# Optimization experiments

Hardware: AMD Instinct MI355X
Metric: run time of the kernel (lower is better)

The kernel has to match this reference:

```python
import jax, jax.numpy as jnp
import numpy as np

T, B, D, H = 512, 64, 1024, 1024
SIGMA = 0.01

def setup_inputs() -> dict:
    key = jax.random.key(0)
    ks = jax.random.split(key, 10)
    w = lambda k, shape: jax.random.normal(k, shape, dtype=jnp.float32) * SIGMA
    return {
        "inputs": jax.random.normal(ks[0], (T, B, D), dtype=jnp.float32),
        "H0": jnp.zeros((B, H), dtype=jnp.float32),
        "C0": jnp.zeros((B, H), dtype=jnp.float32),
        "W_xi": w(ks[1], (D, H)), "W_hi": w(ks[2], (H, H)), "b_i": jnp.zeros((H,), jnp.float32),
        "W_xf": w(ks[3], (D, H)), "W_hf": w(ks[4], (H, H)), "b_f": jnp.zeros((H,), jnp.float32),
        "W_xo": w(ks[5], (D, H)), "W_ho": w(ks[6], (H, H)), "b_o": jnp.zeros((H,), jnp.float32),
        "W_xc": w(ks[7], (D, H)), "W_hc": w(ks[8], (H, H)), "b_c": jnp.zeros((H,), jnp.float32),
    }

def reference(inputs, H0, C0, W_xi, W_hi, b_i, W_xf, W_hf, b_f,
              W_xo, W_ho, b_o, W_xc, W_hc, b_c):
    # Precompute all input-side gate projections in one big GEMM over the
    # full sequence: [T, B, 4H]. Recurrent H-projection stays in the scan.
    Wx = jnp.concatenate([W_xi, W_xf, W_xo, W_xc], axis=1)   # [D, 4H]
    Wh = jnp.concatenate([W_hi, W_hf, W_ho, W_hc], axis=1)   # [H, 4H]
    b  = jnp.concatenate([b_i, b_f, b_o, b_c])                # [4H]
    x_proj = jnp.einsum('tbd,dh->tbh', inputs, Wx) + b        # [T, B, 4H]

    def step(carry, xg):
        h, c = carry
        gates = xg + h @ Wh                                   # [B, 4H]
        i, f, o, g = jnp.split(gates, 4, axis=-1)
        i = jax.nn.sigmoid(i); f = jax.nn.sigmoid(f); o = jax.nn.sigmoid(o)
        c_new = f * c + i * jnp.tanh(g)
        h_new = o * jnp.tanh(c_new)
        return (h_new, c_new), h_new

    (Hf, Cf), outputs = jax.lax.scan(step, (H0, C0), x_proj)
    return outputs, Hf, Cf
```

## Files before the change

### kernel.cpp

```cpp
#include <hip/hip_runtime.h>


typedef unsigned short u16;
typedef unsigned int   u32;
typedef unsigned long long u64;
typedef __attribute__((ext_vector_type(8))) short bf16x8;
typedef __attribute__((ext_vector_type(4))) float f32x4;

__device__ __forceinline__ float bf2f(u16 u) {
    union { u32 i; float f; } v; v.i = ((u32)u) << 16; return v.f;
}
__device__ __forceinline__ u16 f2bf(float f) {
    union { float f; u32 u; } v; v.f = f;
    u32 u = v.u;
    return (u16)((u + 0x7FFFu + ((u >> 16) & 1u)) >> 16);
}
__device__ __forceinline__ float sigm(float x)   { return 1.f / (1.f + __expf(-x)); }
__device__ __forceinline__ float tanh_f(float x) { return 1.f - 2.f / (1.f + __expf(2.f * x)); }

__global__ void k_init(const float* __restrict__ H0,
                       const float* __restrict__ bi, const float* __restrict__ bff,
                       const float* __restrict__ bo, const float* __restrict__ bc,
                       u16* __restrict__ hbuf, float* __restrict__ bias,
                       u32* __restrict__ flags)
{
    int i = blockIdx.x * 256 + threadIdx.x;
#pragma unroll
    for (int r = 0; r < 4; ++r) {
        int idx = i + r * 16384;
        hbuf[idx] = f2bf(H0[idx]);
    }
    if (i < 4096) {
        const float* bp = (i < 1024) ? bi : (i < 2048) ? bff : (i < 3072) ? bo : bc;
        bias[i] = bp[i & 1023];
    }
    if (i < 1024) flags[i] = 0u;
}

__global__ void k_cvt(const float4* __restrict__ in, ushort4* __restrict__ out)
{
    size_t i = (size_t)blockIdx.x * 256 + threadIdx.x;
    float4 v = in[i];
    ushort4 o;
    o.x = f2bf(v.x); o.y = f2bf(v.y); o.z = f2bf(v.z); o.w = f2bf(v.w);
    out[i] = o;
}

__global__ void k_wt(const float* s0, const float* s1, const float* s2, const float* s3,
                     const float* s4, const float* s5, const float* s6, const float* s7,
                     u16* __restrict__ wxT, u16* __restrict__ whT)
{
    const float* srcs[8] = {s0, s1, s2, s3, s4, s5, s6, s7};
    int z = blockIdx.z;
    const float* src = srcs[z];
    u16* dst = (z < 4) ? (wxT + (size_t)z * 1048576) : (whT + (size_t)(z - 4) * 1048576);
    __shared__ float tile[32][33];
    int k0 = blockIdx.x * 32, n0 = blockIdx.y * 32;
    int tx = threadIdx.x, ty = threadIdx.y;
#pragma unroll
    for (int s = 0; s < 4; ++s)
        tile[ty + 8 * s][tx] = src[(size_t)(k0 + ty + 8 * s) * 1024 + n0 + tx];
    __syncthreads();
#pragma unroll
    for (int s = 0; s < 4; ++s)
        dst[(size_t)(n0 + ty + 8 * s) * 1024 + k0 + tx] = f2bf(tile[tx][ty + 8 * s]);
}

__global__ __launch_bounds__(256, 2) void k_gemm(const u16* __restrict__ A,
                                                 const u16* __restrict__ BT,
                                                 u16* __restrict__ C)
{
    __shared__ __attribute__((aligned(16))) u16 lsA[128][64];
    __shared__ __attribute__((aligned(16))) u16 lsB[128][64];
    const int tid  = threadIdx.x;
    const int lane = tid & 63;
    const int wv   = tid >> 6;
    const int wm   = wv >> 1, wn = wv & 1;
    const int m0   = blockIdx.x * 128;
    const int n0   = blockIdx.y * 128;
    const int fr   = lane & 15, fq = lane >> 4;
    const int srow = tid >> 3;
    const int sk8  = tid & 7;

    f32x4 acc[4][4] = {};

    for (int kt = 0; kt < 16; ++kt) {
        const int k0 = kt * 64;
#pragma unroll
        for (int it = 0; it < 4; ++it) {
            int row = srow + it * 32;
            int kg  = (sk8 ^ (row & 7)) * 8;
            uint4 va = *(const uint4*)(A  + (size_t)(m0 + row) * 1024 + k0 + kg);
            uint4 vb = *(const uint4*)(BT + (size_t)(n0 + row) * 1024 + k0 + kg);
            *(uint4*)&lsA[row][sk8 * 8] = va;
            *(uint4*)&lsB[row][sk8 * 8] = vb;
        }
        __syncthreads();
#pragma unroll
        for (int kc = 0; kc < 2; ++kc) {
            const int kb = kc * 32 + 8 * fq;
            bf16x8 af[4], bfv[4];
#pragma unroll
            for (int i = 0; i < 4; ++i) {
                int ra = 64 * wm + 16 * i + fr;
                af[i] = *(const bf16x8*)&lsA[ra][kb ^ ((ra & 7) * 8)];
            }
#pragma unroll
            for (int j = 0; j < 4; ++j) {
                int rb = 64 * wn + 16 * j + fr;
                bfv[j] = *(const bf16x8*)&lsB[rb][kb ^ ((rb & 7) * 8)];
            }
#pragma unroll
            for (int i = 0; i < 4; ++i)
#pragma unroll
                for (int j = 0; j < 4; ++j)
                    acc[i][j] = __builtin_amdgcn_mfma_f32_16x16x32_bf16(af[i], bfv[j], acc[i][j], 0, 0, 0);
        }
        __syncthreads();
    }
#pragma unroll
    for (int i = 0; i < 4; ++i) {
        int grow = m0 + 64 * wm + 16 * i + 4 * fq;
#pragma unroll
        for (int j = 0; j < 4; ++j) {
            int gcol = n0 + 64 * wn + 16 * j + fr;
#pragma unroll
            for (int r = 0; r < 4; ++r)
                C[(size_t)(grow + r) * 4096 + gcol] = f2bf(acc[i][j][r]);
        }
    }
}

__global__ __launch_bounds__(512, 1) void k_scan(const u16* __restrict__ xproj,
                                                 const u16* __restrict__ whT,
                                                 const float* __restrict__ bias,
                                                 const float* __restrict__ C0,
                                                 u16* __restrict__ hbuf,
                                                 u32* __restrict__ flags,
                                                 float* __restrict__ out)
{
    __shared__ __attribute__((aligned(16))) u16   lds_w[64][1024];
    __shared__ __attribute__((aligned(16))) float lds_p[4][4][16][16];

    const int wg  = blockIdx.x;
    const int bg  = wg >> 6;
    const int cg  = wg & 63;
    const int b0  = bg * 16;
    const int j0  = cg * 16;
    const int tid = threadIdx.x;
    const int lane = tid & 63;
    const int wv  = tid >> 6;
    const int fr  = lane & 15;
    const int fq  = lane >> 4;

    for (int it = 0; it < 16; ++it) {
        int idx = tid + it * 512;
        int row = idx >> 7;
        int k8  = idx & 127;
        int gg  = row >> 4, jj = row & 15;
        uint4 v = *((const uint4*)(whT + ((size_t)(gg * 1024 + j0 + jj) << 10)) + k8);
        *(uint4*)&lds_w[row][(k8 * 8) ^ ((row & 7) * 8)] = v;
    }

    const int eb = tid >> 4;
    const int ej = tid & 15;
    float c_state = 0.f;
    float bia[4] = {0.f, 0.f, 0.f, 0.f};
    if (tid < 256) {
        c_state = C0[(size_t)(b0 + eb) * 1024 + j0 + ej];
#pragma unroll
        for (int q = 0; q < 4; ++q) bia[q] = bias[q * 1024 + j0 + ej];
    }
    __syncthreads();

    const int ks = wv;
    u32* fl = flags + bg * 256;

    for (int t = 0; t < 512; ++t) {
        const int p = t & 1;
        const u16* hb = hbuf + (size_t)p * 65536;

        union { bf16x8 v[4]; uint4 q[4]; } afu;
        {
            const u16* hp = hb + (size_t)(b0 + fr) * 1024 + ks * 128 + 8 * fq;
#pragma unroll
            for (int kk = 0; kk < 4; ++kk)
                afu.q[kk] = *(const uint4*)(hp + kk * 32);
        }

        float xg[4] = {0.f, 0.f, 0.f, 0.f};
        if (tid < 256) {
            const u16* xp = xproj + ((size_t)t * 64 + (b0 + eb)) * 4096 + j0 + ej;
#pragma unroll
            for (int q = 0; q < 4; ++q) xg[q] = bf2f(xp[q * 1024]);
        }

        f32x4 acc[4] = {};
#pragma unroll
        for (int g = 0; g < 4; ++g) {
            const int row = g * 16 + fr;
            const int swz = (row & 7) * 8;
#pragma unroll
            for (int kk = 0; kk < 4; ++kk) {
                bf16x8 bv = *(const bf16x8*)&lds_w[row][(ks * 128 + kk * 32 + 8 * fq) ^ swz];
                acc[g] = __builtin_amdgcn_mfma_f32_16x16x32_bf16(afu.v[kk], bv, acc[g], 0, 0, 0);
            }
        }

        if (wv >= 4) {
#pragma unroll
            for (int g = 0; g < 4; ++g)
#pragma unroll
                for (int r = 0; r < 4; ++r)
                    lds_p[wv - 4][g][4 * fq + r][fr] = acc[g][r];
        }
        __syncthreads();
        if (wv < 4) {
#pragma unroll
            for (int g = 0; g < 4; ++g)
#pragma unroll
                for (int r = 0; r < 4; ++r)
                    lds_p[wv][g][4 * fq + r][fr] += acc[g][r];
        }
        __syncthreads();

        if (tid < 256) {
            float gate[4];
#pragma unroll
            for (int q = 0; q < 4; ++q)
                gate[q] = lds_p[0][q][eb][ej] + lds_p[1][q][eb][ej]
                        + lds_p[2][q][eb][ej] + lds_p[3][q][eb][ej] + xg[q] + bia[q];
            float i_ = sigm(gate[0]);
            float f_ = sigm(gate[1]);
            float o_ = sigm(gate[2]);
            float g_ = tanh_f(gate[3]);
            c_state = f_ * c_state + i_ * g_;
            float h_ = o_ * tanh_f(c_state);

            size_t hidx = (size_t)(b0 + eb) * 1024 + j0 + ej;

            u32 lo = (u32)f2bf(h_) | ((u32)f2bf(__shfl_down(h_, 1)) << 16);
            u64 qv = (u64)lo | ((u64)(u32)__shfl_down((int)lo, 2) << 32);
            if ((ej & 3) == 0)
                __hip_atomic_store((u64*)(hbuf + (size_t)(p ^ 1) * 65536 + hidx), qv,
                                   __ATOMIC_RELAXED, __HIP_MEMORY_SCOPE_AGENT);
            asm volatile("s_waitcnt vmcnt(0)" ::: "memory");
            if (lane == 0)
                __hip_atomic_store(fl + cg * 4 + wv, (u32)(t + 1),
                                   __ATOMIC_RELAXED, __HIP_MEMORY_SCOPE_AGENT);

            out[(size_t)t * 65536 + hidx] = h_;
            if (t == 511) {
                out[(size_t)33554432 + hidx] = h_;
                out[(size_t)33554432 + 65536 + hidx] = c_state;
            }
        }

        if (wv == 4) {
            const u64* fp = (const u64*)(fl + lane * 4);
            const u32 tgt = (u32)(t + 1);
            while (true) {
                u64 a = __hip_atomic_load(fp + 0, __ATOMIC_RELAXED, __HIP_MEMORY_SCOPE_AGENT);
                u64 b = __hip_atomic_load(fp + 1, __ATOMIC_RELAXED, __HIP_MEMORY_SCOPE_AGENT);
                bool ok = ((u32)a >= tgt) && ((u32)(a >> 32) >= tgt) &&
                          ((u32)b >= tgt) && ((u32)(b >> 32) >= tgt);
                if (__all(ok)) break;
            }
            __builtin_amdgcn_fence(__ATOMIC_ACQUIRE, "agent");
        }
        __syncthreads();
    }
}

extern "C" void kernel_launch(void* const* d_in, const int* in_sizes, int n_in,
                              void* d_out, int out_size, void* d_ws, size_t ws_size,
                              hipStream_t stream)
{
    const float* inputs = (const float*)d_in[0];
    const float* H0     = (const float*)d_in[1];
    const float* C0     = (const float*)d_in[2];
    const float* Wx[4]  = {(const float*)d_in[3], (const float*)d_in[6],
                           (const float*)d_in[9], (const float*)d_in[12]};
    const float* Wh[4]  = {(const float*)d_in[4], (const float*)d_in[7],
                           (const float*)d_in[10], (const float*)d_in[13]};
    const float* bs[4]  = {(const float*)d_in[5], (const float*)d_in[8],
                           (const float*)d_in[11], (const float*)d_in[14]};

    char* ws = (char*)d_ws;
    u16*  xproj = (u16*)(ws);
    u16*  inb   = (u16*)(ws + 268435456);
    u16*  wxT   = (u16*)(ws + 335544320);
    u16*  whT   = (u16*)(ws + 343932928);
    float* bias = (float*)(ws + 352321536);
    u16*  hbuf  = (u16*)(ws + 352337920);
    u32*  flags = (u32*)(ws + 352600064);
    float* out  = (float*)d_out;

    k_init<<<dim3(64), dim3(256), 0, stream>>>(H0, bs[0], bs[1], bs[2], bs[3], hbuf, bias, flags);
    k_cvt<<<dim3(32768), dim3(256), 0, stream>>>((const float4*)inputs, (ushort4*)inb);
    k_wt<<<dim3(32, 32, 8), dim3(32, 8), 0, stream>>>(Wx[0], Wx[1], Wx[2], Wx[3],
                                                      Wh[0], Wh[1], Wh[2], Wh[3], wxT, whT);
    k_gemm<<<dim3(256, 32), dim3(256), 0, stream>>>(inb, wxT, xproj);
    k_scan<<<dim3(256), dim3(512), 0, stream>>>(xproj, whT, bias, C0, hbuf, flags, out);
}
```

Measured before the change: 3.975 ms.

## Replace per-wave flag polling with per-batch-group atomic counter and tile xproj layout

The per-step cross-workgroup barrier changes. Previously a wave polled 256 per-wave flags. Now each workgroup does a __syncthreads, bumps one per-batch-group counter with atomicAdd, and a single lane spins on it with s_sleep until it reaches (t+1)*64. Separately, the GEMM epilogue writes xproj in a [t][bg][cg][q][16x16] tiled layout, so each scan workgroup's per-step input-gate reads become contiguous 256-element blocks instead of strided 4096-wide rows. The aim is to cut polling traffic and uncoalesced loads on the serial critical path, at the cost of an extra block barrier per step and atomic contention on one counter per group.

Measured after the change: 3.725 ms. 6.3% less time.

```diff
diff --git a/kernel.cpp b/kernel.cpp
--- a/kernel.cpp
+++ b/kernel.cpp
@@ -22,7 +22,7 @@
                        const float* __restrict__ bi, const float* __restrict__ bff,
                        const float* __restrict__ bo, const float* __restrict__ bc,
                        u16* __restrict__ hbuf, float* __restrict__ bias,
-                       u32* __restrict__ flags)
+                       u32* __restrict__ ctr)
 {
     int i = blockIdx.x * 256 + threadIdx.x;
 #pragma unroll
@@ -34,7 +34,7 @@
         const float* bp = (i < 1024) ? bi : (i < 2048) ? bff : (i < 3072) ? bo : bc;
         bias[i] = bp[i & 1023];
     }
-    if (i < 1024) flags[i] = 0u;
+    if (i < 1024) ctr[i] = 0u;
 }
 
 __global__ void k_cvt(const float4* __restrict__ in, ushort4* __restrict__ out)
@@ -124,9 +124,17 @@
 #pragma unroll
         for (int j = 0; j < 4; ++j) {
             int gcol = n0 + 64 * wn + 16 * j + fr;
-#pragma unroll
-            for (int r = 0; r < 4; ++r)
-                C[(size_t)(grow + r) * 4096 + gcol] = f2bf(acc[i][j][r]);
+            int q  = gcol >> 10;
+            int jg = gcol & 1023;
+            int cg = jg >> 4, ej = jg & 15;
+#pragma unroll
+            for (int r = 0; r < 4; ++r) {
+                int m = grow + r;
+                int t = m >> 6, b = m & 63;
+                int bg = b >> 4, eb = b & 15;
+                size_t idx = ((((size_t)t * 4 + bg) * 64 + cg) * 4 + q) * 256 + eb * 16 + ej;
+                C[idx] = f2bf(acc[i][j][r]);
+            }
         }
     }
 }
@@ -136,7 +144,7 @@
                                                  const float* __restrict__ bias,
                                                  const float* __restrict__ C0,
                                                  u16* __restrict__ hbuf,
-                                                 u32* __restrict__ flags,
+                                                 u32* __restrict__ ctr,
                                                  float* __restrict__ out)
 {
     __shared__ __attribute__((aligned(16))) u16   lds_w[64][1024];
@@ -174,7 +182,8 @@
     __syncthreads();
 
     const int ks = wv;
-    u32* fl = flags + bg * 256;
+    u32* ctr_bg = ctr + bg * 64;
+    const u16* xbase = xproj + (((size_t)bg * 64 + cg) * 1024) + eb * 16 + ej;
 
     for (int t = 0; t < 512; ++t) {
         const int p = t & 1;
@@ -190,9 +199,9 @@
 
         float xg[4] = {0.f, 0.f, 0.f, 0.f};
         if (tid < 256) {
-            const u16* xp = xproj + ((size_t)t * 64 + (b0 + eb)) * 4096 + j0 + ej;
-#pragma unroll
-            for (int q = 0; q < 4; ++q) xg[q] = bf2f(xp[q * 1024]);
+            const u16* xp = xbase + (size_t)t * 262144;
+#pragma unroll
+            for (int q = 0; q < 4; ++q) xg[q] = bf2f(xp[q * 256]);
         }
 
         f32x4 acc[4] = {};
@@ -245,9 +254,6 @@
                 __hip_atomic_store((u64*)(hbuf + (size_t)(p ^ 1) * 65536 + hidx), qv,
                                    __ATOMIC_RELAXED, __HIP_MEMORY_SCOPE_AGENT);
             asm volatile("s_waitcnt vmcnt(0)" ::: "memory");
-            if (lane == 0)
-                __hip_atomic_store(fl + cg * 4 + wv, (u32)(t + 1),
-                                   __ATOMIC_RELAXED, __HIP_MEMORY_SCOPE_AGENT);
 
             out[(size_t)t * 65536 + hidx] = h_;
             if (t == 511) {
@@ -256,15 +262,15 @@
             }
         }
 
+        __syncthreads();
+        if (tid == 0)
+            atomicAdd(ctr_bg, 1u);
+
         if (wv == 4) {
-            const u64* fp = (const u64*)(fl + lane * 4);
-            const u32 tgt = (u32)(t + 1);
-            while (true) {
-                u64 a = __hip_atomic_load(fp + 0, __ATOMIC_RELAXED, __HIP_MEMORY_SCOPE_AGENT);
-                u64 b = __hip_atomic_load(fp + 1, __ATOMIC_RELAXED, __HIP_MEMORY_SCOPE_AGENT);
-                bool ok = ((u32)a >= tgt) && ((u32)(a >> 32) >= tgt) &&
-                          ((u32)b >= tgt) && ((u32)(b >> 32) >= tgt);
-                if (__all(ok)) break;
+            if (lane == 0) {
+                const u32 tgt = (u32)(t + 1) * 64u;
+                while (__hip_atomic_load(ctr_bg, __ATOMIC_RELAXED, __HIP_MEMORY_SCOPE_AGENT) < tgt)
+                    __builtin_amdgcn_s_sleep(1);
             }
             __builtin_amdgcn_fence(__ATOMIC_ACQUIRE, "agent");
         }
@@ -293,13 +299,13 @@
     u16*  whT   = (u16*)(ws + 343932928);
     float* bias = (float*)(ws + 352321536);
     u16*  hbuf  = (u16*)(ws + 352337920);
-    u32*  flags = (u32*)(ws + 352600064);
+    u32*  ctr   = (u32*)(ws + 352600064);
     float* out  = (float*)d_out;
 
-    k_init<<<dim3(64), dim3(256), 0, stream>>>(H0, bs[0], bs[1], bs[2], bs[3], hbuf, bias, flags);
+    k_init<<<dim3(64), dim3(256), 0, stream>>>(H0, bs[0], bs[1], bs[2], bs[3], hbuf, bias, ctr);
     k_cvt<<<dim3(32768), dim3(256), 0, stream>>>((const float4*)inputs, (ushort4*)inb);
     k_wt<<<dim3(32, 32, 8), dim3(32, 8), 0, stream>>>(Wx[0], Wx[1], Wx[2], Wx[3],
                                                       Wh[0], Wh[1], Wh[2], Wh[3], wxT, whT);
     k_gemm<<<dim3(256, 32), dim3(256), 0, stream>>>(inb, wxT, xproj);
-    k_scan<<<dim3(256), dim3(512), 0, stream>>>(xproj, whT, bias, C0, hbuf, flags, out);
-}
+    k_scan<<<dim3(256), dim3(512), 0, stream>>>(xproj, whT, bias, C0, hbuf, ctr, out);
+}
```
